# Optimization experiments

Hardware: AMD Instinct MI355X
Metric: run time of the kernel (lower is better)

## Reference

```python
import jax, jax.numpy as jnp
import numpy as np

NBITS = 4
N_NODES = 8192
IN_F = 1024
OUT_F = 1024


def _act_quant(x, alpha, b):
    # clamp only from above (no min clamp), uniform quantize to 2^b-1 levels
    n = float(2 ** b - 1)
    xd = x / alpha
    xc = jnp.minimum(xd, 1.0)
    xq = jnp.round(xc * n) / n
    return xq * alpha


def _weight_quant(w, alpha, b):
    # symmetric clamp to [-1,1], sign-magnitude uniform quant with 2^b-1 levels
    n = float(2 ** b - 1)
    wd = w / alpha
    wc = jnp.clip(wd, -1.0, 1.0)
    wq = jnp.round(jnp.abs(wc) * n) / n * jnp.sign(wc)
    return wq * alpha


def setup_inputs() -> dict:
    key = jax.random.key(0)
    k1, k2, k3 = jax.random.split(key, 3)
    stdv = 1.0 / np.sqrt(OUT_F)
    inp = {
        "input": jax.random.uniform(k1, (N_NODES, IN_F), dtype=jnp.float32),
        "adj": jax.random.uniform(k2, (N_NODES, N_NODES), dtype=jnp.float32),
        "adj_scaling_factor": jnp.float32(2.0),
        "weight": jax.random.uniform(k3, (IN_F, OUT_F), minval=-stdv, maxval=stdv, dtype=jnp.float32),
        "wgt_alpha": jnp.float32(3.0),
        "act_alpha": jnp.float32(1.0),
        "act_alpha2": jnp.float32(1.0),
    }
    return inp


def reference(input, adj, adj_scaling_factor, weight, wgt_alpha, act_alpha, act_alpha2):
    bit = NBITS
    wb = bit - 1  # weight_quantize_fn uses w_bit - 1 internal bits
    # normalize weight by detached mean/std (unbiased std, matching torch)
    mean = jax.lax.stop_gradient(jnp.mean(weight))
    std = jax.lax.stop_gradient(jnp.std(weight, ddof=1))
    w_norm = (weight - mean) / std
    weight_q = _weight_quant(w_norm, wgt_alpha, wb)

    x = _act_quant(input, act_alpha, bit)
    wgt_delta = wgt_alpha / (2 ** (bit - 1) - 1)
    act_delta = act_alpha / (2 ** bit - 1)
    # int-domain GEMM expressed with inline dequant scaling, as in the source
    support = jnp.matmul(x / act_delta, weight_q / wgt_delta)
    support = support * act_delta * wgt_delta
    support = jax.nn.relu(support)

    support_q = _act_quant(support, act_alpha2, bit)
    support_delta = act_alpha2 / (2 ** bit - 1)
    output = jnp.matmul(adj / adj_scaling_factor, support_q / support_delta)
    return output * adj_scaling_factor * support_delta
```

## Files before the change

### kernel.cpp

```cpp
#include <hip/hip_runtime.h>


#define AS_G __attribute__((address_space(1)))
#define AS_L __attribute__((address_space(3)))

typedef int i32x4 __attribute__((ext_vector_type(4)));
typedef char c8 __attribute__((ext_vector_type(8)));
typedef char c16 __attribute__((ext_vector_type(16)));

static __device__ __forceinline__ void gload_lds16(const char* g, char* l) {
  __builtin_amdgcn_global_load_lds((const AS_G unsigned int*)g,
                                   (AS_L unsigned int*)l, 16, 0, 0);
}

__global__ void pre_kernel(const float* __restrict__ w, double* __restrict__ stats,
                           const float* __restrict__ x, char* __restrict__ xq,
                           const float* __restrict__ alpha_p, int wn, int xn) {
  if (blockIdx.x < 256) {
    double s = 0.0, ss = 0.0;
    for (int i = (blockIdx.x * 256 + threadIdx.x) * 4; i < wn; i += 256 * 256 * 4) {
      float4 v = *(const float4*)&w[i];
      s += (double)v.x + (double)v.y + (double)v.z + (double)v.w;
      ss += (double)v.x * v.x + (double)v.y * v.y + (double)v.z * v.z + (double)v.w * v.w;
    }
#pragma unroll
    for (int off = 32; off > 0; off >>= 1) {
      s  += __shfl_down(s, off);
      ss += __shfl_down(ss, off);
    }
    if ((threadIdx.x & 63) == 0) {
      atomicAdd(&stats[0], s);
      atomicAdd(&stats[1], ss);
    }
  } else {
    int i = ((blockIdx.x - 256) * 256 + threadIdx.x) * 8;
    if (i >= xn) return;
    const float alpha = *alpha_p;
    float4 v0 = *(const float4*)&x[i];
    float4 v1 = *(const float4*)&x[i + 4];
    c8 o;
    o[0] = (char)(int)rintf(fminf(v0.x / alpha, 1.f) * 15.f);
    o[1] = (char)(int)rintf(fminf(v0.y / alpha, 1.f) * 15.f);
    o[2] = (char)(int)rintf(fminf(v0.z / alpha, 1.f) * 15.f);
    o[3] = (char)(int)rintf(fminf(v0.w / alpha, 1.f) * 15.f);
    o[4] = (char)(int)rintf(fminf(v1.x / alpha, 1.f) * 15.f);
    o[5] = (char)(int)rintf(fminf(v1.y / alpha, 1.f) * 15.f);
    o[6] = (char)(int)rintf(fminf(v1.z / alpha, 1.f) * 15.f);
    o[7] = (char)(int)rintf(fminf(v1.w / alpha, 1.f) * 15.f);
    *(c8*)&xq[i] = o;
  }
}

__global__ void wquant_kernel(const float* __restrict__ w, char* __restrict__ wt,
                              const double* __restrict__ stats,
                              const float* __restrict__ alpha_p) {
  int idx = blockIdx.x * 256 + threadIdx.x;
  const double cnt = 1048576.0;
  const double mean = stats[0] / cnt;
  const double var = (stats[1] - stats[0] * mean) / (cnt - 1.0);
  const float meanf = (float)mean;
  const float stdf = (float)sqrt(var);
  const float alpha = *alpha_p;
  const int n = idx >> 10;
  const int k = idx & 1023;
  float wn = (w[(size_t)k * 1024 + n] - meanf) / stdf;
  float wc = fminf(fmaxf(wn / alpha, -1.f), 1.f);
  wt[idx] = (char)(int)copysignf(rintf(fabsf(wc) * 7.f), wc);
}

template <bool RELUQ, bool AF32>
static __device__ __forceinline__ void gemm_body(
    const void* __restrict__ Av, const char* __restrict__ B, void* __restrict__ Cv,
    float* __restrict__ outp,
    const int M, const int N, const int LDK, const int Kspan, const int zidx,
    const float* s0p, const float* s1p, const float* s2p) {
  __shared__ __align__(16) char As[2][128 * 64];
  __shared__ __align__(16) char Bs[2][128 * 64];

  const int tid = threadIdx.x;
  const int lane = tid & 63;
  const int wv = tid >> 6;
  const int wm = wv >> 1, wn = wv & 1;
  const int m0 = blockIdx.x * 128, n0 = blockIdx.y * 128;
  const int kz = zidx * Kspan;

  const int srow = tid >> 2;
  const int scol = (((tid & 3) + 4 - ((tid >> 3) & 3)) & 3) * 16;
  const int frow = tid >> 1;
  const int ft = (tid & 1) * 2;
  const int fsh = (tid >> 2) & 3;

  i32x4 acc[4][4];
#pragma unroll
  for (int i = 0; i < 4; ++i)
#pragma unroll
    for (int j = 0; j < 4; ++j) acc[i][j] = (i32x4){0, 0, 0, 0};

  const int lrow = lane & 15;
  const int q16 = (((lane >> 4) + (lrow >> 1)) & 3) * 16;

  auto stage = [&](int b, int kt) {
    if (AF32) {
      const float* Af = (const float*)Av;
      const float* src = Af + (size_t)(m0 + frow) * LDK + kt + (tid & 1) * 32;
      c16 p0, p1;
#pragma unroll
      for (int j = 0; j < 4; ++j) {
        float4 v = *(const float4*)(src + 4 * j);
        p0[4 * j + 0] = (char)(int)rintf(v.x * 127.f);
        p0[4 * j + 1] = (char)(int)rintf(v.y * 127.f);
        p0[4 * j + 2] = (char)(int)rintf(v.z * 127.f);
        p0[4 * j + 3] = (char)(int)rintf(v.w * 127.f);
      }
#pragma unroll
      for (int j = 0; j < 4; ++j) {
        float4 v = *(const float4*)(src + 16 + 4 * j);
        p1[4 * j + 0] = (char)(int)rintf(v.x * 127.f);
        p1[4 * j + 1] = (char)(int)rintf(v.y * 127.f);
        p1[4 * j + 2] = (char)(int)rintf(v.z * 127.f);
        p1[4 * j + 3] = (char)(int)rintf(v.w * 127.f);
      }
      *(c16*)&As[b][frow * 64 + (((ft + 0) + fsh) & 3) * 16] = p0;
      *(c16*)&As[b][frow * 64 + (((ft + 1) + fsh) & 3) * 16] = p1;
    } else {
      const char* Ab = (const char*)Av;
      gload_lds16(Ab + (size_t)(m0 + srow) * LDK + kt + scol, &As[b][wv * 1024]);
      gload_lds16(Ab + (size_t)(m0 + 64 + srow) * LDK + kt + scol,
                  &As[b][4096 + wv * 1024]);
    }
    gload_lds16(B + (size_t)(n0 + srow) * LDK + kt + scol, &Bs[b][wv * 1024]);
    gload_lds16(B + (size_t)(n0 + 64 + srow) * LDK + kt + scol,
                &Bs[b][4096 + wv * 1024]);
  };

  const int nt = Kspan / 64;
  stage(0, kz);
  __syncthreads();

  for (int t = 0; t < nt; ++t) {
    const int cur = t & 1;
    if (t + 1 < nt) stage(cur ^ 1, kz + (t + 1) * 64);

    i32x4 af[4], bfr[4];
#pragma unroll
    for (int mi = 0; mi < 4; ++mi)
      af[mi] = *(const i32x4*)&As[cur][(wm * 64 + mi * 16 + lrow) * 64 + q16];
#pragma unroll
    for (int ni = 0; ni < 4; ++ni)
      bfr[ni] = *(const i32x4*)&Bs[cur][(wn * 64 + ni * 16 + lrow) * 64 + q16];
#pragma unroll
    for (int mi = 0; mi < 4; ++mi)
#pragma unroll
      for (int ni = 0; ni < 4; ++ni)
        acc[mi][ni] =
            __builtin_amdgcn_mfma_i32_16x16x64_i8(af[mi], bfr[ni], acc[mi][ni], 0, 0, 0);

    __syncthreads();
  }

  const int qr = (lane >> 4) * 4;
  if (RELUQ) {
    const float d_act = *s0p / 15.f;
    const float d_wgt = *s1p / 7.f;
    const float a2 = *s2p;
    char* Ct = (char*)Cv;
#pragma unroll
    for (int mi = 0; mi < 4; ++mi) {
      const int mb = m0 + wm * 64 + mi * 16 + qr;
#pragma unroll
      for (int ni = 0; ni < 4; ++ni) {
        const int n = n0 + wn * 64 + ni * 16 + lrow;
        char4 pk;
#pragma unroll
        for (int r = 0; r < 4; ++r) {
          float s = (float)acc[mi][ni][r] * d_act * d_wgt;
          s = fmaxf(s, 0.f);
          float xc = fminf(s / a2, 1.f);
          ((char*)&pk)[r] = (char)(int)rintf(xc * 15.f);
        }
        *(char4*)&Ct[(size_t)n * M + mb] = pk;
      }
    }
  } else {
    const float sc = (*s2p) * (1.f / 15.f) * (1.f / 127.f);
#pragma unroll
    for (int mi = 0; mi < 4; ++mi) {
      const int mb = m0 + wm * 64 + mi * 16 + qr;
#pragma unroll
      for (int ni = 0; ni < 4; ++ni) {
        const int n = n0 + wn * 64 + ni * 16 + lrow;
#pragma unroll
        for (int r = 0; r < 4; ++r)
          atomicAdd(&outp[(size_t)(mb + r) * N + n], (float)acc[mi][ni][r] * sc);
      }
    }
  }
}

template <bool RELUQ, bool AF32>
__global__ __launch_bounds__(256, 4) void gemm_i8_kernel(
    const void* __restrict__ Av, const char* __restrict__ B, void* __restrict__ Cv,
    float* __restrict__ outp,
    const int M, const int N, const int LDK, const int Kspan,
    const float* __restrict__ s0p, const float* __restrict__ s1p,
    const float* __restrict__ s2p) {
  gemm_body<RELUQ, AF32>(Av, B, Cv, outp, M, N, LDK, Kspan, blockIdx.z,
                         s0p, s1p, s2p);
}

__global__ __launch_bounds__(256, 4) void gemm1_adjq_kernel(
    const void* __restrict__ Av, const char* __restrict__ B, void* __restrict__ Cv,
    const float* __restrict__ s0p, const float* __restrict__ s1p,
    const float* __restrict__ s2p,
    const float* __restrict__ adj, char* __restrict__ adjq, long long an) {
  if (blockIdx.z == 1) {
    const long long bid = (long long)blockIdx.y * gridDim.x + blockIdx.x;
    for (long long i = (bid * 256 + threadIdx.x) * 16; i < an;
         i += (long long)512 * 256 * 16) {
      c16 r;
#pragma unroll
      for (int j = 0; j < 4; ++j) {
        float4 v = *(const float4*)&adj[i + 4 * j];
        r[4 * j + 0] = (char)(int)rintf(v.x * 127.f);
        r[4 * j + 1] = (char)(int)rintf(v.y * 127.f);
        r[4 * j + 2] = (char)(int)rintf(v.z * 127.f);
        r[4 * j + 3] = (char)(int)rintf(v.w * 127.f);
      }
      *(c16*)&adjq[i] = r;
    }
    return;
  }
  gemm_body<true, false>(Av, B, Cv, nullptr, 8192, 1024, 1024, 1024, 0,
                         s0p, s1p, s2p);
}

__global__ __launch_bounds__(512, 2) void gemm2_8ph_kernel(
    const char* __restrict__ A, const char* __restrict__ B,
    float* __restrict__ outp, const float* __restrict__ s2p) {
  __shared__ __align__(16) char As[3][256 * 64];
  __shared__ __align__(16) char Bs[3][256 * 64];

  const int tid = threadIdx.x;
  const int lane = tid & 63;
  const int wv = tid >> 6;
  const int wm = wv >> 2, wn = wv & 3;
  const int m0 = blockIdx.x * 256, n0 = blockIdx.y * 256;
  const int kz = blockIdx.z * 4096;

  const int lrow = lane & 15;
  const int q16 = (((lane >> 4) + (lrow >> 1)) & 3) * 16;
  const int srow = tid >> 2;
  const int scol = (((tid & 3) + 4 - ((tid >> 3) & 3)) & 3) * 16;
  const int wdst = wv * 1024;

  i32x4 acc[8][4];
#pragma unroll
  for (int i = 0; i < 8; ++i)
#pragma unroll
    for (int j = 0; j < 4; ++j) acc[i][j] = (i32x4){0, 0, 0, 0};

  auto stage = [&](int b, int kt) {
    const char* Ap = A + (size_t)(m0 + srow) * 8192 + kt + scol;
    gload_lds16(Ap, &As[b][wdst]);
    gload_lds16(Ap + (size_t)128 * 8192, &As[b][8192 + wdst]);
    const char* Bp = B + (size_t)(n0 + srow) * 8192 + kt + scol;
    gload_lds16(Bp, &Bs[b][wdst]);
    gload_lds16(Bp + (size_t)128 * 8192, &Bs[b][8192 + wdst]);
  };

  const int nt = 64;
  stage(0, kz);
  stage(1, kz + 64);
  asm volatile("s_waitcnt vmcnt(4)" ::: "memory");
  __builtin_amdgcn_s_barrier();

  for (int t = 0; t < nt; ++t) {
    const int cur = t % 3;
    if (t + 2 < nt) stage((t + 2) % 3, kz + (t + 2) * 64);

    i32x4 bf[4];
#pragma unroll
    for (int ni = 0; ni < 4; ++ni)
      bf[ni] = *(const i32x4*)&Bs[cur][(wn * 64 + ni * 16 + lrow) * 64 + q16];

#pragma unroll
    for (int g = 0; g < 4; ++g) {
      i32x4 a0 = *(const i32x4*)&As[cur][(wm * 128 + (2 * g) * 16 + lrow) * 64 + q16];
      i32x4 a1 = *(const i32x4*)&As[cur][(wm * 128 + (2 * g + 1) * 16 + lrow) * 64 + q16];
      __builtin_amdgcn_s_setprio(1);
#pragma unroll
      for (int ni = 0; ni < 4; ++ni) {
        acc[2 * g][ni] =
            __builtin_amdgcn_mfma_i32_16x16x64_i8(a0, bf[ni], acc[2 * g][ni], 0, 0, 0);
        acc[2 * g + 1][ni] =
            __builtin_amdgcn_mfma_i32_16x16x64_i8(a1, bf[ni], acc[2 * g + 1][ni], 0, 0, 0);
      }
      __builtin_amdgcn_s_setprio(0);
    }

    if (t + 2 < nt) {
      asm volatile("s_waitcnt vmcnt(4)" ::: "memory");
    } else {
      asm volatile("s_waitcnt vmcnt(0)" ::: "memory");
    }
    __builtin_amdgcn_s_barrier();
  }

  const float sc = (*s2p) * (1.f / 15.f) * (1.f / 127.f);
  const int qr = (lane >> 4) * 4;
#pragma unroll
  for (int mi = 0; mi < 8; ++mi) {
    const int mb = m0 + wm * 128 + mi * 16 + qr;
#pragma unroll
    for (int ni = 0; ni < 4; ++ni) {
      const int n = n0 + wn * 64 + ni * 16 + lrow;
#pragma unroll
      for (int r = 0; r < 4; ++r)
        atomicAdd(&outp[(size_t)(mb + r) * 1024 + n], (float)acc[mi][ni][r] * sc);
    }
  }
}

extern "C" void kernel_launch(void* const* d_in, const int* in_sizes, int n_in,
                              void* d_out, int out_size, void* d_ws, size_t ws_size,
                              hipStream_t stream) {
  const float* input  = (const float*)d_in[0];
  const float* adj    = (const float*)d_in[1];
  const float* weight = (const float*)d_in[3];
  const float* wgt_alpha  = (const float*)d_in[4];
  const float* act_alpha  = (const float*)d_in[5];
  const float* act_alpha2 = (const float*)d_in[6];
  float* out = (float*)d_out;

  constexpr int NN = 8192, INF = 1024, OUTF = 1024;
  constexpr size_t MB = 1024 * 1024;
  constexpr size_t HDR = 64 * 1024;

  char* ws = (char*)d_ws;
  double* stats = (double*)ws;
  char* WtI  = ws + HDR;
  char* XqI  = ws + HDR + 1 * MB;
  char* StI  = ws + HDR + 9 * MB;
  char* AdjQ = ws + HDR + 17 * MB;
  const size_t need = HDR + 81 * MB;

  hipMemsetAsync(stats, 0, 256, stream);
  hipMemsetAsync(out, 0, (size_t)NN * OUTF * sizeof(float), stream);

  pre_kernel<<<256 + (NN * INF / 8) / 256, 256, 0, stream>>>(
      weight, stats, input, XqI, act_alpha, INF * OUTF, NN * INF);
  wquant_kernel<<<(INF * OUTF) / 256, 256, 0, stream>>>(weight, WtI, stats, wgt_alpha);

  if (ws_size >= need) {
    gemm1_adjq_kernel<<<dim3(NN / 128, OUTF / 128, 2), 256, 0, stream>>>(
        XqI, WtI, StI, act_alpha, wgt_alpha, act_alpha2, adj, AdjQ, (long long)NN * NN);
    gemm2_8ph_kernel<<<dim3(NN / 256, OUTF / 256, 2), 512, 0, stream>>>(
        AdjQ, StI, out, act_alpha2);
  } else {
    gemm_i8_kernel<true, false><<<dim3(NN / 128, OUTF / 128, 1), 256, 0, stream>>>(
        XqI, WtI, StI, nullptr, NN, OUTF, INF, INF,
        act_alpha, wgt_alpha, act_alpha2);
    gemm_i8_kernel<false, true><<<dim3(NN / 128, OUTF / 128, 2), 256, 0, stream>>>(
        adj, StI, nullptr, out, NN, OUTF, NN, NN / 2, nullptr, nullptr, act_alpha2);
  }
}
```

Before: 558.7 us.

## Shrink gemm2 tile to 128x256 with double buffering and fold output zeroing

The adjacency GEMM kernel moves from a 256x256 tile with triple-buffered LDS and hand-tuned waitcnt pipelining to a 128x256 tile with simple double buffering and __syncthreads, doubling the grid and targeting four blocks per CU. Separately, the output memset is replaced by extra blocks in pre_kernel that zero the output, removing one memset launch. The smaller tile raises occupancy but lowers data reuse per block, adds more atomic split-K traffic per element, and drops the deeper prefetch and setprio scheduling.

```diff
diff --git a/kernel.cpp b/kernel.cpp
--- a/kernel.cpp
+++ b/kernel.cpp
@@ -15,7 +15,8 @@
 
 __global__ void pre_kernel(const float* __restrict__ w, double* __restrict__ stats,
                            const float* __restrict__ x, char* __restrict__ xq,
-                           const float* __restrict__ alpha_p, int wn, int xn) {
+                           const float* __restrict__ alpha_p,
+                           float* __restrict__ outz, int wn, int xn) {
   if (blockIdx.x < 256) {
     double s = 0.0, ss = 0.0;
     for (int i = (blockIdx.x * 256 + threadIdx.x) * 4; i < wn; i += 256 * 256 * 4) {
@@ -32,7 +33,7 @@
       atomicAdd(&stats[0], s);
       atomicAdd(&stats[1], ss);
     }
-  } else {
+  } else if (blockIdx.x < 256 + 4096) {
     int i = ((blockIdx.x - 256) * 256 + threadIdx.x) * 8;
     if (i >= xn) return;
     const float alpha = *alpha_p;
@@ -48,6 +49,13 @@
     o[6] = (char)(int)rintf(fminf(v1.z / alpha, 1.f) * 15.f);
     o[7] = (char)(int)rintf(fminf(v1.w / alpha, 1.f) * 15.f);
     *(c8*)&xq[i] = o;
+  } else {
+    const size_t i = ((size_t)(blockIdx.x - 4352) * 256 + threadIdx.x) * 16;
+    const float4 z = {0.f, 0.f, 0.f, 0.f};
+    *(float4*)&outz[i]      = z;
+    *(float4*)&outz[i + 4]  = z;
+    *(float4*)&outz[i + 8]  = z;
+    *(float4*)&outz[i + 12] = z;
   }
 }
 
@@ -234,83 +242,67 @@
                          s0p, s1p, s2p);
 }
 
-__global__ __launch_bounds__(512, 2) void gemm2_8ph_kernel(
+__global__ __launch_bounds__(512, 4) void gemm2_kernel(
     const char* __restrict__ A, const char* __restrict__ B,
     float* __restrict__ outp, const float* __restrict__ s2p) {
-  __shared__ __align__(16) char As[3][256 * 64];
-  __shared__ __align__(16) char Bs[3][256 * 64];
+  __shared__ __align__(16) char As[2][128 * 64];
+  __shared__ __align__(16) char Bs[2][256 * 64];
 
   const int tid = threadIdx.x;
   const int lane = tid & 63;
   const int wv = tid >> 6;
   const int wm = wv >> 2, wn = wv & 3;
-  const int m0 = blockIdx.x * 256, n0 = blockIdx.y * 256;
+  const int m0 = blockIdx.x * 128, n0 = blockIdx.y * 256;
   const int kz = blockIdx.z * 4096;
 
   const int lrow = lane & 15;
   const int q16 = (((lane >> 4) + (lrow >> 1)) & 3) * 16;
   const int srow = tid >> 2;
   const int scol = (((tid & 3) + 4 - ((tid >> 3) & 3)) & 3) * 16;
-  const int wdst = wv * 1024;
-
-  i32x4 acc[8][4];
-#pragma unroll
-  for (int i = 0; i < 8; ++i)
+
+  i32x4 acc[4][4];
+#pragma unroll
+  for (int i = 0; i < 4; ++i)
 #pragma unroll
     for (int j = 0; j < 4; ++j) acc[i][j] = (i32x4){0, 0, 0, 0};
 
   auto stage = [&](int b, int kt) {
-    const char* Ap = A + (size_t)(m0 + srow) * 8192 + kt + scol;
-    gload_lds16(Ap, &As[b][wdst]);
-    gload_lds16(Ap + (size_t)128 * 8192, &As[b][8192 + wdst]);
+    gload_lds16(A + (size_t)(m0 + srow) * 8192 + kt + scol, &As[b][wv * 1024]);
     const char* Bp = B + (size_t)(n0 + srow) * 8192 + kt + scol;
-    gload_lds16(Bp, &Bs[b][wdst]);
-    gload_lds16(Bp + (size_t)128 * 8192, &Bs[b][8192 + wdst]);
+    gload_lds16(Bp, &Bs[b][wv * 1024]);
+    gload_lds16(Bp + (size_t)128 * 8192, &Bs[b][8192 + wv * 1024]);
   };
 
   const int nt = 64;
   stage(0, kz);
-  stage(1, kz + 64);
-  asm volatile("s_waitcnt vmcnt(4)" ::: "memory");
-  __builtin_amdgcn_s_barrier();
+  __syncthreads();
 
   for (int t = 0; t < nt; ++t) {
-    const int cur = t % 3;
-    if (t + 2 < nt) stage((t + 2) % 3, kz + (t + 2) * 64);
-
-    i32x4 bf[4];
+    const int cur = t & 1;
+    if (t + 1 < nt) stage(cur ^ 1, kz + (t + 1) * 64);
+
+    i32x4 af[4], bfr[4];
+#pragma unroll
+    for (int mi = 0; mi < 4; ++mi)
+      af[mi] = *(const i32x4*)&As[cur][(wm * 64 + mi * 16 + lrow) * 64 + q16];
 #pragma unroll
     for (int ni = 0; ni < 4; ++ni)
-      bf[ni] = *(const i32x4*)&Bs[cur][(wn * 64 + ni * 16 + lrow) * 64 + q16];
-
-#pragma unroll
-    for (int g = 0; g < 4; ++g) {
-      i32x4 a0 = *(const i32x4*)&As[cur][(wm * 128 + (2 * g) * 16 + lrow) * 64 + q16];
-      i32x4 a1 = *(const i32x4*)&As[cur][(wm * 128 + (2 * g + 1) * 16 + lrow) * 64 + q16];
-      __builtin_amdgcn_s_setprio(1);
-#pragma unroll
-      for (int ni = 0; ni < 4; ++ni) {
-        acc[2 * g][ni] =
-            __builtin_amdgcn_mfma_i32_16x16x64_i8(a0, bf[ni], acc[2 * g][ni], 0, 0, 0);
-        acc[2 * g + 1][ni] =
-            __builtin_amdgcn_mfma_i32_16x16x64_i8(a1, bf[ni], acc[2 * g + 1][ni], 0, 0, 0);
-      }
-      __builtin_amdgcn_s_setprio(0);
-    }
-
-    if (t + 2 < nt) {
-      asm volatile("s_waitcnt vmcnt(4)" ::: "memory");
-    } else {
-      asm volatile("s_waitcnt vmcnt(0)" ::: "memory");
-    }
-    __builtin_amdgcn_s_barrier();
+      bfr[ni] = *(const i32x4*)&Bs[cur][(wn * 64 + ni * 16 + lrow) * 64 + q16];
+#pragma unroll
+    for (int mi = 0; mi < 4; ++mi)
+#pragma unroll
+      for (int ni = 0; ni < 4; ++ni)
+        acc[mi][ni] =
+            __builtin_amdgcn_mfma_i32_16x16x64_i8(af[mi], bfr[ni], acc[mi][ni], 0, 0, 0);
+
+    __syncthreads();
   }
 
   const float sc = (*s2p) * (1.f / 15.f) * (1.f / 127.f);
   const int qr = (lane >> 4) * 4;
 #pragma unroll
-  for (int mi = 0; mi < 8; ++mi) {
-    const int mb = m0 + wm * 128 + mi * 16 + qr;
+  for (int mi = 0; mi < 4; ++mi) {
+    const int mb = m0 + wm * 64 + mi * 16 + qr;
 #pragma unroll
     for (int ni = 0; ni < 4; ++ni) {
       const int n = n0 + wn * 64 + ni * 16 + lrow;
@@ -345,16 +337,15 @@
   const size_t need = HDR + 81 * MB;
 
   hipMemsetAsync(stats, 0, 256, stream);
-  hipMemsetAsync(out, 0, (size_t)NN * OUTF * sizeof(float), stream);
-
-  pre_kernel<<<256 + (NN * INF / 8) / 256, 256, 0, stream>>>(
-      weight, stats, input, XqI, act_alpha, INF * OUTF, NN * INF);
+
+  pre_kernel<<<256 + 4096 + 2048, 256, 0, stream>>>(
+      weight, stats, input, XqI, act_alpha, out, INF * OUTF, NN * INF);
   wquant_kernel<<<(INF * OUTF) / 256, 256, 0, stream>>>(weight, WtI, stats, wgt_alpha);
 
   if (ws_size >= need) {
     gemm1_adjq_kernel<<<dim3(NN / 128, OUTF / 128, 2), 256, 0, stream>>>(
         XqI, WtI, StI, act_alpha, wgt_alpha, act_alpha2, adj, AdjQ, (long long)NN * NN);
-    gemm2_8ph_kernel<<<dim3(NN / 256, OUTF / 256, 2), 512, 0, stream>>>(
+    gemm2_kernel<<<dim3(NN / 128, OUTF / 256, 2), 512, 0, stream>>>(
         AdjQ, StI, out, act_alpha2);
   } else {
     gemm_i8_kernel<true, false><<<dim3(NN / 128, OUTF / 128, 1), 256, 0, stream>>>(
```

After: 552.3 us. About the same (-1.1%).
